# Kernel optimization log

Measured on AMD Instinct MI355X. Metric: run time of the kernel, lower is better.

Reference implementation:

```python
import jax, jax.numpy as jnp
import numpy as np

M, L, Q = 512, 256, 21


def setup_inputs() -> dict:
    key = jax.random.key(0)
    k1, k2, k3 = jax.random.split(key, 3)
    # one-hot encoded sequences (M, L, q)
    X_idx = jax.random.randint(k1, (M, L), 0, Q)
    X_oh = jax.nn.one_hot(X_idx, Q, dtype=jnp.float32)
    h_pos = 0.01 * jax.random.normal(k2, (L, Q), dtype=jnp.float32)
    J = 0.01 * jax.random.normal(k3, (L, L, Q, Q), dtype=jnp.float32)
    return {"X_oh": X_oh, "h_pos": h_pos, "J": J}


def reference(X_oh, h_pos, J):
    # z[m,i,a] = h[i,a] + sum_{j<i} sum_b J[i,j,b,a] * X[m,j,b]
    # (matches torch einsum 'mpq,pqr->mpr' over tril-gathered blocks)
    L_, q_ = h_pos.shape
    i_idx, j_idx = jnp.tril_indices(L_, k=-1)          # (P,), strictly lower, i sorted
    J_blocks = J[i_idx, j_idx]                          # (P, q, q)
    X_blocks = X_oh[:, j_idx]                           # (M, P, q)
    contrib = jnp.einsum('mpb,pba->mpa', X_blocks, J_blocks)  # (M, P, q)
    # scatter-add contributions to their target position i (sorted segments)
    agg = jax.ops.segment_sum(
        jnp.swapaxes(contrib, 0, 1),                    # (P, M, q)
        i_idx, num_segments=L_, indices_are_sorted=True
    )                                                   # (L, M, q)
    return h_pos[None, :, :] + jnp.swapaxes(agg, 0, 1)  # (M, L, q)
```

## Files before the change

kernel.cpp:

```cpp
#include <hip/hip_runtime.h>

#define Q_DIM 21
#define BLKB  1764
#define WINB  1792
#define SLOT  2304
#define NBUF  6
#define DEPTH 3

#define GLD(src, dst, sz) __builtin_amdgcn_global_load_lds( \
    (const __attribute__((address_space(1))) void*)(src),   \
    (__attribute__((address_space(3))) void*)(dst), sz, 0, 0)

__global__ __launch_bounds__(64) void ardca_prep(const float* __restrict__ X_oh,
                                                 unsigned short* __restrict__ Xt) {
  int w = blockIdx.x;
  int lane = threadIdx.x;
  const float* base = X_oh + (size_t)w * (32 * Q_DIM);
  int rowbase = w * 32;
#pragma unroll
  for (int p = 0; p < 11; ++p) {
    int f = p * 63 + lane;
    float v = (lane < 63 && f < 672) ? base[f] : 0.0f;
    unsigned long long mask = __ballot(v > 0.5f);
    if (lane < 3) {
      int rloc = 3 * p + lane;
      if (rloc < 32) {
        unsigned int bits = (unsigned int)((mask >> (21 * lane)) & 0x1FFFFFu);
        int x = bits ? __builtin_ctz(bits) : 0;
        int rr = rowbase + rloc;
        int m = rr >> 8, j = rr & 255;
        Xt[j * 512 + m] = (unsigned short)(x * 84);
      }
    }
  }
}

template <int USE_XT>
__global__ __launch_bounds__(512, 4) void ardca_main(const float* __restrict__ Jm,
                                                     const float* __restrict__ h,
                                                     const unsigned short* __restrict__ Xt,
                                                     const float* __restrict__ X_oh,
                                                     float* __restrict__ out) {
  alignas(16) __shared__ char lds[NBUF * SLOT];
  int b = blockIdx.x;
  int i, mh;
  if (b < 256) { i = b; mh = 0; }
  else { int x = b - 256; i = 248 - (x & ~7) + (x & 7); mh = 1; }
  int tid = threadIdx.x;
  int ml = tid & 255;
  int ah = tid >> 8;
  int m = mh * 256 + ml;

  const char* Jrow = (const char*)Jm + (size_t)i * (256ull * BLKB);
  const char* XtB  = (const char*)Xt;

  const float* hp = h + i * Q_DIM + ah * 12;
  float acc[12];
#pragma unroll
  for (int k = 0; k < 12; ++k)
    acc[k] = (k < 9 || ah == 0) ? hp[k] : 0.0f;

  auto STAGE = [&](int j) {
    char* buf = lds + (j % NBUF) * SLOT;
    unsigned bb = (unsigned)j * BLKB;
    const char* src = Jrow + (bb & ~15u);
    if (tid < 112) GLD(src + tid * 16, buf + tid * 16, 16);
    if (USE_XT) {
      if (tid >= 128 && tid < 160)
        GLD(XtB + j * 1024 + mh * 512 + (tid - 128) * 16,
            buf + WINB + (tid - 128) * 16, 16);
    }
  };

  auto CONSUME = [&](int j) {
    const char* buf = lds + (j % NBUF) * SLOT;
    int off;
    if (USE_XT) {
      off = *(const unsigned short*)(buf + WINB + 2 * ml);
    } else {
      const float* p = X_oh + ((size_t)m * 256 + j) * Q_DIM;
      int x = 0;
#pragma unroll
      for (int a = 0; a < Q_DIM; ++a) x = (p[a] > 0.5f) ? a : x;
      off = x * 84;
    }
    const float* row = (const float*)(buf + ((j & 3) << 2) + off + ah * 48);
#pragma unroll
    for (int k = 0; k < 12; ++k) acc[k] += row[k];
  };

  int P = (i < DEPTH) ? i : DEPTH;
  for (int j = 0; j < P; ++j) STAGE(j);
  int jt = i - DEPTH; if (jt < 0) jt = 0;

#pragma unroll 1
  for (int j = 0; j < jt; ++j) {
    STAGE(j + DEPTH);
    if (USE_XT) asm volatile("s_waitcnt vmcnt(3)" ::: "memory");
    else        asm volatile("s_waitcnt vmcnt(0)" ::: "memory");
    __builtin_amdgcn_sched_barrier(0);
    __builtin_amdgcn_s_barrier();
    CONSUME(j);
  }
  asm volatile("s_waitcnt vmcnt(0)" ::: "memory");
  __builtin_amdgcn_sched_barrier(0);
  __builtin_amdgcn_s_barrier();
#pragma unroll 1
  for (int j = jt; j < i; ++j) CONSUME(j);

  float* o = out + ((size_t)m * 256 + i) * Q_DIM + ah * 12;
  if (ah == 0) {
#pragma unroll
    for (int k = 0; k < 12; ++k) o[k] = acc[k];
  } else {
#pragma unroll
    for (int k = 0; k < 9; ++k) o[k] = acc[k];
  }
}

extern "C" void kernel_launch(void* const* d_in, const int* in_sizes, int n_in,
                              void* d_out, int out_size, void* d_ws, size_t ws_size,
                              hipStream_t stream) {
  const float* X_oh = (const float*)d_in[0];
  const float* h    = (const float*)d_in[1];
  const float* Jm   = (const float*)d_in[2];
  float* out        = (float*)d_out;
  unsigned short* Xt = (unsigned short*)d_ws;

  if (ws_size >= 262144) {
    ardca_prep<<<4096, 64, 0, stream>>>(X_oh, Xt);
    ardca_main<1><<<512, 512, 0, stream>>>(Jm, h, Xt, X_oh, out);
  } else {
    ardca_main<0><<<512, 512, 0, stream>>>(Jm, h, Xt, X_oh, out);
  }
}
```

Before: 223.0 us.

## Split each row's j-range into 32-wide chunks across blocks with atomic accumulation

Each output row i is split into chunks of 32 source positions j, with each chunk handled by its own block, giving a grid of about 2290 blocks instead of 512. Partial sums are combined with atomic adds into an output that is zeroed first with a memset. The change targets the load imbalance of the triangular workload, where a block's work grows with i, and raises the occupancy hint to 8. In exchange it adds a memset, float atomics with nondeterministic summation order, and pipeline prologue and epilogue cost for every short chunk.

```diff
diff --git a/kernel.cpp b/kernel.cpp
--- a/kernel.cpp
+++ b/kernel.cpp
@@ -6,6 +6,9 @@
 #define SLOT  2304
 #define NBUF  6
 #define DEPTH 3
+#define CH    32
+#define NQ    1145
+#define GRIDH 1152
 
 #define GLD(src, dst, sz) __builtin_amdgcn_global_load_lds( \
     (const __attribute__((address_space(1))) void*)(src),   \
@@ -36,16 +39,39 @@
 }
 
 template <int USE_XT>
-__global__ __launch_bounds__(512, 4) void ardca_main(const float* __restrict__ Jm,
+__global__ __launch_bounds__(512, 8) void ardca_main(const float* __restrict__ Jm,
                                                      const float* __restrict__ h,
                                                      const unsigned short* __restrict__ Xt,
                                                      const float* __restrict__ X_oh,
                                                      float* __restrict__ out) {
   alignas(16) __shared__ char lds[NBUF * SLOT];
   int b = blockIdx.x;
-  int i, mh;
-  if (b < 256) { i = b; mh = 0; }
-  else { int x = b - 256; i = 248 - (x & ~7) + (x & 7); mh = 1; }
+  int mh = (b >= GRIDH) ? 1 : 0;
+  int q = b - mh * GRIDH;
+  if (q >= NQ) return;
+  int g, r;
+  if      (q <  33) { g = 0; r = q;       }
+  else if (q <  97) { g = 1; r = q - 33;  }
+  else if (q < 193) { g = 2; r = q - 97;  }
+  else if (q < 321) { g = 3; r = q - 193; }
+  else if (q < 481) { g = 4; r = q - 321; }
+  else if (q < 673) { g = 5; r = q - 481; }
+  else if (q < 897) { g = 6; r = q - 673; }
+  else              { g = 7; r = q - 897; }
+  int i, c;
+  switch (g) {
+    case 0:  i = r;              c = 0;     break;
+    case 1:  i = 33  + (r >> 1); c = r & 1; break;
+    case 2:  i = 65  + r / 3;    c = r % 3; break;
+    case 3:  i = 97  + (r >> 2); c = r & 3; break;
+    case 4:  i = 129 + r / 5;    c = r % 5; break;
+    case 5:  i = 161 + r / 6;    c = r % 6; break;
+    case 6:  i = 193 + r / 7;    c = r % 7; break;
+    default: i = 225 + (r >> 3); c = r & 7; break;
+  }
+  int jlo = c * CH;
+  int jhi = jlo + CH; if (jhi > i) jhi = i;
+
   int tid = threadIdx.x;
   int ml = tid & 255;
   int ah = tid >> 8;
@@ -54,11 +80,15 @@
   const char* Jrow = (const char*)Jm + (size_t)i * (256ull * BLKB);
   const char* XtB  = (const char*)Xt;
 
-  const float* hp = h + i * Q_DIM + ah * 12;
   float acc[12];
+  if (c == 0) {
+    const float* hp = h + i * Q_DIM + ah * 12;
 #pragma unroll
-  for (int k = 0; k < 12; ++k)
-    acc[k] = (k < 9 || ah == 0) ? hp[k] : 0.0f;
+    for (int k = 0; k < 12; ++k) acc[k] = (k < 9 || ah == 0) ? hp[k] : 0.0f;
+  } else {
+#pragma unroll
+    for (int k = 0; k < 12; ++k) acc[k] = 0.0f;
+  }
 
   auto STAGE = [&](int j) {
     char* buf = lds + (j % NBUF) * SLOT;
@@ -86,15 +116,16 @@
     }
     const float* row = (const float*)(buf + ((j & 3) << 2) + off + ah * 48);
 #pragma unroll
-    for (int k = 0; k < 12; ++k) acc[k] += row[k];
+    for (int k = 0; k < 12; ++k)
+      if (ah == 0 || k < 9) acc[k] += row[k];
   };
 
-  int P = (i < DEPTH) ? i : DEPTH;
-  for (int j = 0; j < P; ++j) STAGE(j);
-  int jt = i - DEPTH; if (jt < 0) jt = 0;
+  int P = jhi - jlo; if (P > DEPTH) P = DEPTH;
+  for (int j = jlo; j < jlo + P; ++j) STAGE(j);
+  int jt = jhi - DEPTH; if (jt < jlo) jt = jlo;
 
 #pragma unroll 1
-  for (int j = 0; j < jt; ++j) {
+  for (int j = jlo; j < jt; ++j) {
     STAGE(j + DEPTH);
     if (USE_XT) asm volatile("s_waitcnt vmcnt(3)" ::: "memory");
     else        asm volatile("s_waitcnt vmcnt(0)" ::: "memory");
@@ -106,16 +137,12 @@
   __builtin_amdgcn_sched_barrier(0);
   __builtin_amdgcn_s_barrier();
 #pragma unroll 1
-  for (int j = jt; j < i; ++j) CONSUME(j);
+  for (int j = jt; j < jhi; ++j) CONSUME(j);
 
   float* o = out + ((size_t)m * 256 + i) * Q_DIM + ah * 12;
-  if (ah == 0) {
 #pragma unroll
-    for (int k = 0; k < 12; ++k) o[k] = acc[k];
-  } else {
-#pragma unroll
-    for (int k = 0; k < 9; ++k) o[k] = acc[k];
-  }
+  for (int k = 0; k < 12; ++k)
+    if (ah == 0 || k < 9) unsafeAtomicAdd(&o[k], acc[k]);
 }
 
 extern "C" void kernel_launch(void* const* d_in, const int* in_sizes, int n_in,
@@ -127,10 +154,11 @@
   float* out        = (float*)d_out;
   unsigned short* Xt = (unsigned short*)d_ws;
 
+  hipMemsetAsync(d_out, 0, (size_t)out_size * sizeof(float), stream);
   if (ws_size >= 262144) {
     ardca_prep<<<4096, 64, 0, stream>>>(X_oh, Xt);
-    ardca_main<1><<<512, 512, 0, stream>>>(Jm, h, Xt, X_oh, out);
+    ardca_main<1><<<2 * GRIDH, 512, 0, stream>>>(Jm, h, Xt, X_oh, out);
   } else {
-    ardca_main<0><<<512, 512, 0, stream>>>(Jm, h, Xt, X_oh, out);
+    ardca_main<0><<<2 * GRIDH, 512, 0, stream>>>(Jm, h, Xt, X_oh, out);
   }
 }
```

Measured after the change: 827.4 us. 271% more time.
